# Kernel tuning notes

Measured on AMD Instinct MI355X. Metric: run time of the kernel, lower is better.

## Reference

```python
import jax, jax.numpy as jnp
import numpy as np

BATCH = 4096
DIM = 512
NOISE_POWER = 1.0


def setup_inputs() -> dict:
    key = jax.random.key(0)
    k1, k2 = jax.random.split(key)
    info = jax.random.normal(k1, (BATCH, DIM), dtype=jnp.float32)
    codewords = jax.random.normal(k2, (BATCH, DIM), dtype=jnp.float32)
    sigma = (NOISE_POWER * jnp.eye(DIM, dtype=jnp.float32))
    return {"info": info, "codewords": codewords, "sigma": sigma}


def _gmm_entropy_upper(mu, sigma):
    """Kolchinsky-style upper bound on Gaussian-mixture entropy.

    Faithful to tensor_entropy_gauss_mix_upper: pairwise Mahalanobis
    quadratic form exponent[i, j] = -0.5 * (mu_i - mu_j)^T Sig^-1 (mu_i - mu_j),
    computed via the Gram-matrix expansion instead of materializing the
    [B*B, dim] repeat/tile intermediates.
    """
    B, dim = mu.shape
    sig_inv = jnp.linalg.inv(sigma)
    A = mu @ sig_inv                      # [B, dim]
    q = jnp.sum(A * mu, axis=1)           # [B] diagonal quadratic terms
    G = A @ mu.T                          # [B, B]  mu_i Sig^-1 mu_j^T
    # expo[i, j] = -0.5*(q_i + q_j - G[i,j] - G[j,i])
    expo = -0.5 * (q[:, None] + q[None, :] - G - G.T)
    lse = jax.nn.logsumexp(expo, axis=1)  # [B], over mixture components j
    weight = 1.0 / B
    factor_log = -(dim / 2.0) * jnp.log(2.0 * jnp.pi * sigma[0, 0])
    log_inner = jnp.log(weight) + factor_log + lse
    entropy = dim / 2.0 - jnp.sum(weight * log_inner)
    return entropy


def reference(info, codewords, sigma):
    # Original call: info, codewords = inputs; info_codewords = codewords
    # (info is unpacked but unused). h_z and h_zm both use codewords.
    h_z = _gmm_entropy_upper(codewords, sigma)
    h_zm = _gmm_entropy_upper(codewords, sigma)
    return jnp.stack([h_z, h_zm])
```

## Files before the change

### kernel.cpp

```cpp
#include <hip/hip_runtime.h>
#include <math.h>

#define NB 4096
#define ND 512
#define TILE 128
#define BK 32

typedef __bf16 bf16x8 __attribute__((ext_vector_type(8)));
typedef __bf16 bf16x4 __attribute__((ext_vector_type(4)));
typedef float floatx4 __attribute__((ext_vector_type(4)));

__device__ inline void async_load16(const void* g, void* l) {
    __builtin_amdgcn_global_load_lds((const __attribute__((address_space(1))) void*)g,
                                     (__attribute__((address_space(3))) void*)l, 16, 0, 0);
}

__global__ __launch_bounds__(128) void prep_kernel(const float* __restrict__ mu,
                                                   __bf16* __restrict__ mubf,
                                                   float* __restrict__ hq,
                                                   float* __restrict__ sumexp) {
    const int row = blockIdx.x;
    const int t = threadIdx.x;
    const float4 v = ((const float4*)(mu + (size_t)row * ND))[t];
    __bf16 b0 = (__bf16)v.x, b1 = (__bf16)v.y, b2 = (__bf16)v.z, b3 = (__bf16)v.w;
    bf16x4 pack; pack[0] = b0; pack[1] = b1; pack[2] = b2; pack[3] = b3;
    ((bf16x4*)(mubf + (size_t)row * ND))[t] = pack;
    float f0 = (float)b0, f1 = (float)b1, f2 = (float)b2, f3 = (float)b3;
    float sq = f0 * f0 + f1 * f1 + f2 * f2 + f3 * f3;
    #pragma unroll
    for (int off = 32; off > 0; off >>= 1) sq += __shfl_down(sq, off, 64);
    __shared__ float red[2];
    if ((t & 63) == 0) red[t >> 6] = sq;
    __syncthreads();
    if (t == 0) {
        hq[row] = 0.5f * (red[0] + red[1]);
        sumexp[row] = 0.0f;
    }
}

__global__ __launch_bounds__(256) void gram_lse_kernel(const __bf16* __restrict__ mubf,
                                                       const float* __restrict__ hq,
                                                       const float* __restrict__ sigma,
                                                       float* __restrict__ sumexp) {
    __shared__ alignas(16) __bf16 As[TILE * BK];
    __shared__ alignas(16) __bf16 Bs[TILE * BK];

    const int t = threadIdx.x;
    const int row0 = blockIdx.y * TILE;
    const int col0 = blockIdx.x * TILE;
    const int wave = t >> 6;
    const int lane = t & 63;
    const int r16 = lane & 15;
    const int quad = lane >> 4;
    const int rw = (wave >> 1) * 64;
    const int cw = (wave & 1) * 64;

    const int srow = t >> 2;
    const int skoff = (t & 3) * 8;
    const __bf16* gA0 = mubf + (size_t)(row0 + srow) * ND + skoff;
    const __bf16* gA1 = gA0 + (size_t)64 * ND;
    const __bf16* gB0 = mubf + (size_t)(col0 + srow) * ND + skoff;
    const __bf16* gB1 = gB0 + (size_t)64 * ND;
    __bf16* lA0 = &As[t * 8];
    __bf16* lA1 = &As[2048 + t * 8];
    __bf16* lB0 = &Bs[t * 8];
    __bf16* lB1 = &Bs[2048 + t * 8];

    floatx4 acc[4][4];
    #pragma unroll
    for (int i = 0; i < 4; i++)
        #pragma unroll
        for (int j = 0; j < 4; j++) {
            floatx4 z = {0.f, 0.f, 0.f, 0.f};
            acc[i][j] = z;
        }

    for (int kk = 0; kk < ND; kk += BK) {
        __syncthreads();
        async_load16(gA0 + kk, lA0);
        async_load16(gA1 + kk, lA1);
        async_load16(gB0 + kk, lB0);
        async_load16(gB1 + kk, lB1);
        __syncthreads();

        bf16x8 a[4], b[4];
        #pragma unroll
        for (int i = 0; i < 4; i++)
            a[i] = *(const bf16x8*)&As[(rw + i * 16 + r16) * BK + quad * 8];
        #pragma unroll
        for (int j = 0; j < 4; j++)
            b[j] = *(const bf16x8*)&Bs[(cw + j * 16 + r16) * BK + quad * 8];
        #pragma unroll
        for (int i = 0; i < 4; i++)
            #pragma unroll
            for (int j = 0; j < 4; j++)
                acc[i][j] = __builtin_amdgcn_mfma_f32_16x16x32_bf16(a[i], b[j], acc[i][j], 0, 0, 0);
    }

    const float inv_s = 1.0f / sigma[0];
    float hqc[4];
    #pragma unroll
    for (int j = 0; j < 4; j++) hqc[j] = hq[col0 + cw + j * 16 + r16];

    #pragma unroll
    for (int i = 0; i < 4; i++) {
        #pragma unroll
        for (int r = 0; r < 4; r++) {
            const int row = row0 + rw + i * 16 + quad * 4 + r;
            const float hr = hq[row];
            float rs = 0.0f;
            #pragma unroll
            for (int j = 0; j < 4; j++) {
                const float g = acc[i][j][r];
                rs += __expf((g - hr - hqc[j]) * inv_s);
            }
            rs += __shfl_xor(rs, 1, 64);
            rs += __shfl_xor(rs, 2, 64);
            rs += __shfl_xor(rs, 4, 64);
            rs += __shfl_xor(rs, 8, 64);
            if (r16 == 0) atomicAdd(&sumexp[row], rs);
        }
    }
}

__global__ __launch_bounds__(256) void finalize_kernel(const float* __restrict__ sumexp,
                                                       const float* __restrict__ sigma,
                                                       float* __restrict__ out) {
    const int t = threadIdx.x;
    float local = 0.0f;
    for (int i = t; i < NB; i += 256) local += logf(sumexp[i]);
    #pragma unroll
    for (int off = 32; off > 0; off >>= 1) local += __shfl_down(local, off, 64);
    __shared__ float red[4];
    if ((t & 63) == 0) red[t >> 6] = local;
    __syncthreads();
    if (t == 0) {
        const float tot = red[0] + red[1] + red[2] + red[3];
        const double s = (double)sigma[0];
        const double ent = (double)(ND / 2)
                         + log((double)NB)
                         + (double)(ND / 2) * log(2.0 * M_PI * s)
                         - (double)tot / (double)NB;
        out[0] = (float)ent;
        out[1] = (float)ent;
    }
}

extern "C" void kernel_launch(void* const* d_in, const int* in_sizes, int n_in,
                              void* d_out, int out_size, void* d_ws, size_t ws_size,
                              hipStream_t stream) {
    (void)in_sizes; (void)n_in; (void)out_size; (void)ws_size;
    const float* codewords = (const float*)d_in[1];
    const float* sigma     = (const float*)d_in[2];
    float* out = (float*)d_out;

    char* ws = (char*)d_ws;
    __bf16* mubf  = (__bf16*)ws;
    float*  hq    = (float*)(ws + (size_t)NB * ND * 2);
    float*  sumexp = hq + NB;

    prep_kernel<<<NB, 128, 0, stream>>>(codewords, mubf, hq, sumexp);
    dim3 grid(NB / TILE, NB / TILE);
    gram_lse_kernel<<<grid, 256, 0, stream>>>(mubf, hq, sigma, sumexp);
    finalize_kernel<<<1, 256, 0, stream>>>(sumexp, sigma, out);
}
```

Baseline: 116.1 us.

## Exploit Gram symmetry with triangular tile grid and fuse finalize via last-block counter

Computes only the upper-triangular tiles of the symmetric Gram matrix. Each off-diagonal tile adds its exponentials to both the row sums and the column sums, which roughly halves the MFMA and load work. Diagonal tiles reuse the A tile as B. The finalize kernel is folded into the gram kernel through a global atomic counter, so the last block computes the entropy, and prep now handles one row per wave. The costs are extra column atomics, a threadfence in every block, and a serial tail reduction inside the last block.

```diff
diff --git a/kernel.cpp b/kernel.cpp
--- a/kernel.cpp
+++ b/kernel.cpp
@@ -5,9 +5,10 @@
 #define ND 512
 #define TILE 128
 #define BK 32
+#define NT (NB / TILE)
+#define NBLK (NT * (NT + 1) / 2)
 
 typedef __bf16 bf16x8 __attribute__((ext_vector_type(8)));
-typedef __bf16 bf16x4 __attribute__((ext_vector_type(4)));
 typedef float floatx4 __attribute__((ext_vector_type(4)));
 
 __device__ inline void async_load16(const void* g, void* l) {
@@ -15,39 +16,53 @@
                                      (__attribute__((address_space(3))) void*)l, 16, 0, 0);
 }
 
-__global__ __launch_bounds__(128) void prep_kernel(const float* __restrict__ mu,
+__global__ __launch_bounds__(256) void prep_kernel(const float* __restrict__ mu,
                                                    __bf16* __restrict__ mubf,
                                                    float* __restrict__ hq,
-                                                   float* __restrict__ sumexp) {
-    const int row = blockIdx.x;
+                                                   float* __restrict__ sumexp,
+                                                   unsigned* __restrict__ counter) {
     const int t = threadIdx.x;
-    const float4 v = ((const float4*)(mu + (size_t)row * ND))[t];
-    __bf16 b0 = (__bf16)v.x, b1 = (__bf16)v.y, b2 = (__bf16)v.z, b3 = (__bf16)v.w;
-    bf16x4 pack; pack[0] = b0; pack[1] = b1; pack[2] = b2; pack[3] = b3;
-    ((bf16x4*)(mubf + (size_t)row * ND))[t] = pack;
-    float f0 = (float)b0, f1 = (float)b1, f2 = (float)b2, f3 = (float)b3;
-    float sq = f0 * f0 + f1 * f1 + f2 * f2 + f3 * f3;
+    const int wave = t >> 6, lane = t & 63;
+    const int row = blockIdx.x * 4 + wave;
+    const float4* src = (const float4*)(mu + (size_t)row * ND) + lane * 2;
+    const float4 v0 = src[0], v1 = src[1];
+    bf16x8 pack;
+    pack[0] = (__bf16)v0.x; pack[1] = (__bf16)v0.y;
+    pack[2] = (__bf16)v0.z; pack[3] = (__bf16)v0.w;
+    pack[4] = (__bf16)v1.x; pack[5] = (__bf16)v1.y;
+    pack[6] = (__bf16)v1.z; pack[7] = (__bf16)v1.w;
+    ((bf16x8*)(mubf + (size_t)row * ND))[lane] = pack;
+    float sq = 0.0f;
+    #pragma unroll
+    for (int e = 0; e < 8; e++) { float f = (float)pack[e]; sq += f * f; }
     #pragma unroll
     for (int off = 32; off > 0; off >>= 1) sq += __shfl_down(sq, off, 64);
-    __shared__ float red[2];
-    if ((t & 63) == 0) red[t >> 6] = sq;
-    __syncthreads();
-    if (t == 0) {
-        hq[row] = 0.5f * (red[0] + red[1]);
+    if (lane == 0) {
+        hq[row] = 0.5f * sq;
         sumexp[row] = 0.0f;
     }
+    if (blockIdx.x == 0 && t == 0) *counter = 0u;
 }
 
 __global__ __launch_bounds__(256) void gram_lse_kernel(const __bf16* __restrict__ mubf,
                                                        const float* __restrict__ hq,
                                                        const float* __restrict__ sigma,
-                                                       float* __restrict__ sumexp) {
+                                                       float* __restrict__ sumexp,
+                                                       unsigned* __restrict__ counter,
+                                                       float* __restrict__ out) {
     __shared__ alignas(16) __bf16 As[TILE * BK];
     __shared__ alignas(16) __bf16 Bs[TILE * BK];
 
+    int b = blockIdx.x;
+    int ti = (int)((sqrt(8.0 * (double)b + 1.0) - 1.0) * 0.5);
+    while ((ti + 1) * (ti + 2) / 2 <= b) ti++;
+    while (ti * (ti + 1) / 2 > b) ti--;
+    const int tj = b - ti * (ti + 1) / 2;
+    const bool isDiag = (ti == tj);
+    const int row0 = ti * TILE;
+    const int col0 = tj * TILE;
+
     const int t = threadIdx.x;
-    const int row0 = blockIdx.y * TILE;
-    const int col0 = blockIdx.x * TILE;
     const int wave = t >> 6;
     const int lane = t & 63;
     const int r16 = lane & 15;
@@ -65,6 +80,7 @@
     __bf16* lA1 = &As[2048 + t * 8];
     __bf16* lB0 = &Bs[t * 8];
     __bf16* lB1 = &Bs[2048 + t * 8];
+    const __bf16* Bsrc = isDiag ? As : Bs;
 
     floatx4 acc[4][4];
     #pragma unroll
@@ -79,22 +95,24 @@
         __syncthreads();
         async_load16(gA0 + kk, lA0);
         async_load16(gA1 + kk, lA1);
-        async_load16(gB0 + kk, lB0);
-        async_load16(gB1 + kk, lB1);
+        if (!isDiag) {
+            async_load16(gB0 + kk, lB0);
+            async_load16(gB1 + kk, lB1);
+        }
         __syncthreads();
 
-        bf16x8 a[4], b[4];
+        bf16x8 a[4], bb[4];
         #pragma unroll
         for (int i = 0; i < 4; i++)
             a[i] = *(const bf16x8*)&As[(rw + i * 16 + r16) * BK + quad * 8];
         #pragma unroll
         for (int j = 0; j < 4; j++)
-            b[j] = *(const bf16x8*)&Bs[(cw + j * 16 + r16) * BK + quad * 8];
+            bb[j] = *(const bf16x8*)&Bsrc[(cw + j * 16 + r16) * BK + quad * 8];
         #pragma unroll
         for (int i = 0; i < 4; i++)
             #pragma unroll
             for (int j = 0; j < 4; j++)
-                acc[i][j] = __builtin_amdgcn_mfma_f32_16x16x32_bf16(a[i], b[j], acc[i][j], 0, 0, 0);
+                acc[i][j] = __builtin_amdgcn_mfma_f32_16x16x32_bf16(a[i], bb[j], acc[i][j], 0, 0, 0);
     }
 
     const float inv_s = 1.0f / sigma[0];
@@ -102,6 +120,7 @@
     #pragma unroll
     for (int j = 0; j < 4; j++) hqc[j] = hq[col0 + cw + j * 16 + r16];
 
+    float cs[4] = {0.f, 0.f, 0.f, 0.f};
     #pragma unroll
     for (int i = 0; i < 4; i++) {
         #pragma unroll
@@ -111,8 +130,9 @@
             float rs = 0.0f;
             #pragma unroll
             for (int j = 0; j < 4; j++) {
-                const float g = acc[i][j][r];
-                rs += __expf((g - hr - hqc[j]) * inv_s);
+                const float v = __expf((acc[i][j][r] - hr - hqc[j]) * inv_s);
+                rs += v;
+                cs[j] += v;
             }
             rs += __shfl_xor(rs, 1, 64);
             rs += __shfl_xor(rs, 2, 64);
@@ -121,28 +141,41 @@
             if (r16 == 0) atomicAdd(&sumexp[row], rs);
         }
     }
-}
+    if (!isDiag) {
+        #pragma unroll
+        for (int j = 0; j < 4; j++) {
+            float c = cs[j];
+            c += __shfl_xor(c, 16, 64);
+            c += __shfl_xor(c, 32, 64);
+            if (quad == 0) atomicAdd(&sumexp[col0 + cw + j * 16 + r16], c);
+        }
+    }
 
-__global__ __launch_bounds__(256) void finalize_kernel(const float* __restrict__ sumexp,
-                                                       const float* __restrict__ sigma,
-                                                       float* __restrict__ out) {
-    const int t = threadIdx.x;
-    float local = 0.0f;
-    for (int i = t; i < NB; i += 256) local += logf(sumexp[i]);
-    #pragma unroll
-    for (int off = 32; off > 0; off >>= 1) local += __shfl_down(local, off, 64);
-    __shared__ float red[4];
-    if ((t & 63) == 0) red[t >> 6] = local;
+    __threadfence();
     __syncthreads();
-    if (t == 0) {
-        const float tot = red[0] + red[1] + red[2] + red[3];
-        const double s = (double)sigma[0];
-        const double ent = (double)(ND / 2)
-                         + log((double)NB)
-                         + (double)(ND / 2) * log(2.0 * M_PI * s)
-                         - (double)tot / (double)NB;
-        out[0] = (float)ent;
-        out[1] = (float)ent;
+    __shared__ unsigned done;
+    if (t == 0)
+        done = __hip_atomic_fetch_add(counter, 1u, __ATOMIC_ACQ_REL, __HIP_MEMORY_SCOPE_AGENT);
+    __syncthreads();
+    if (done == NBLK - 1) {
+        float local = 0.0f;
+        for (int i = t; i < NB; i += 256)
+            local += logf(__hip_atomic_load(&sumexp[i], __ATOMIC_RELAXED, __HIP_MEMORY_SCOPE_AGENT));
+        #pragma unroll
+        for (int off = 32; off > 0; off >>= 1) local += __shfl_down(local, off, 64);
+        __shared__ float fred[4];
+        if ((t & 63) == 0) fred[t >> 6] = local;
+        __syncthreads();
+        if (t == 0) {
+            const double tot = (double)fred[0] + fred[1] + fred[2] + fred[3];
+            const double s = (double)sigma[0];
+            const double ent = (double)(ND / 2)
+                             + log((double)NB)
+                             + (double)(ND / 2) * log(2.0 * M_PI * s)
+                             - tot / (double)NB;
+            out[0] = (float)ent;
+            out[1] = (float)ent;
+        }
     }
 }
 
@@ -155,12 +188,11 @@
     float* out = (float*)d_out;
 
     char* ws = (char*)d_ws;
-    __bf16* mubf  = (__bf16*)ws;
-    float*  hq    = (float*)(ws + (size_t)NB * ND * 2);
+    __bf16* mubf   = (__bf16*)ws;
+    float*  hq     = (float*)(ws + (size_t)NB * ND * 2);
     float*  sumexp = hq + NB;
+    unsigned* counter = (unsigned*)(sumexp + NB);
 
-    prep_kernel<<<NB, 128, 0, stream>>>(codewords, mubf, hq, sumexp);
-    dim3 grid(NB / TILE, NB / TILE);
-    gram_lse_kernel<<<grid, 256, 0, stream>>>(mubf, hq, sigma, sumexp);
-    finalize_kernel<<<1, 256, 0, stream>>>(sumexp, sigma, out);
+    prep_kernel<<<NB / 4, 256, 0, stream>>>(codewords, mubf, hq, sumexp, counter);
+    gram_lse_kernel<<<NBLK, 256, 0, stream>>>(mubf, hq, sigma, sumexp, counter, out);
 }
```

After: 127.7 us. 10.0% more time.
